# Kernel optimization log

Hardware: AMD Instinct MI355X
Metric: run time of the kernel (lower is better)

## Reference

```python
import jax, jax.numpy as jnp
import numpy as np

TAU = 0.5
EPS = 1e-8


def setup_inputs() -> dict:
    key = jax.random.key(0)
    k1, k2 = jax.random.split(key)
    N, D = 200000, 512
    z_pos = jax.random.normal(k1, (N, D), dtype=jnp.float32)
    W = jax.random.normal(k2, (D, D), dtype=jnp.float32) * (1.0 / np.sqrt(D))
    b = jnp.zeros((D,), dtype=jnp.float32)
    return {"z_pos": z_pos, "W": W, "b": b}


def reference(z_pos, W, b):
    # sample_centroid: softmax-weighted centroid (computed on detached embeddings)
    h = jax.lax.stop_gradient(z_pos)
    init_c = h.mean(axis=0)                              # [D]
    d2 = jnp.sum((h - init_c[None, :]) ** 2, axis=1)     # [N]
    w = jax.nn.softmax(-d2 / TAU)                        # [N]
    c = jnp.sum(h * w[:, None], axis=0)                  # [D]

    # SimNet: dist = 1 - cosine_similarity(proj(x), c)
    x_proj = z_pos @ W.T + b                             # [N, D]
    x_norm = jnp.maximum(jnp.linalg.norm(x_proj, axis=-1), EPS)  # [N]
    c_norm = jnp.maximum(jnp.linalg.norm(c), EPS)
    cos = (x_proj @ c) / (x_norm * c_norm)               # [N]
    dist = 1.0 - cos
    return dist
```

## Files before the change

kernel.cpp:

```cpp
#include <hip/hip_runtime.h>
#include <hip/hip_bf16.h>
#include <math.h>

#define DD 512
#define EPSF 1e-8f
#define BM 64
#define BK 32

typedef __bf16 bf16_t;
typedef __bf16 bf16x4 __attribute__((ext_vector_type(4)));
typedef __bf16 bf16x8 __attribute__((ext_vector_type(8)));
typedef float f32x4 __attribute__((ext_vector_type(4)));

__global__ void k_convW(const float* __restrict__ W, bf16_t* __restrict__ Wb) {
    int i = blockIdx.x * blockDim.x + threadIdx.x;
    float4 v = ((const float4*)W)[i];
    bf16x4 o;
    o[0] = (bf16_t)v.x; o[1] = (bf16_t)v.y; o[2] = (bf16_t)v.z; o[3] = (bf16_t)v.w;
    ((bf16x4*)Wb)[i] = o;
}

__global__ void k_colsum(const float* __restrict__ z, float* __restrict__ part, int N) {
    int t = threadIdx.x;
    int b = blockIdx.x;
    const float2* z2 = (const float2*)z;
    float2 acc = make_float2(0.f, 0.f);
    #pragma unroll 4
    for (int r = b; r < N; r += gridDim.x) {
        float2 v = z2[(size_t)r * (DD / 2) + t];
        acc.x += v.x; acc.y += v.y;
    }
    part[(size_t)b * DD + 2 * t]     = acc.x;
    part[(size_t)b * DD + 2 * t + 1] = acc.y;
}

__global__ void k_wcolsum(const float* __restrict__ z, const float* __restrict__ d2,
                          const float* __restrict__ d2min, const float* __restrict__ sinv,
                          float* __restrict__ part, int N) {
    int t = threadIdx.x;
    int b = blockIdx.x;
    float m  = d2min[0];
    float is = sinv[0];
    const float2* z2 = (const float2*)z;
    float2 acc = make_float2(0.f, 0.f);
    #pragma unroll 2
    for (int r = b; r < N; r += gridDim.x) {
        float w = expf(-2.0f * (d2[r] - m)) * is;
        float2 v = z2[(size_t)r * (DD / 2) + t];
        acc.x += w * v.x; acc.y += w * v.y;
    }
    part[(size_t)b * DD + 2 * t]     = acc.x;
    part[(size_t)b * DD + 2 * t + 1] = acc.y;
}

__global__ void k_reduce1024(const float* __restrict__ part, float* __restrict__ outv, float scale) {
    __shared__ float sm[256];
    int j = blockIdx.x;
    int t = threadIdx.x;
    float s = part[(size_t)t * DD + j] + part[(size_t)(t + 256) * DD + j]
            + part[(size_t)(t + 512) * DD + j] + part[(size_t)(t + 768) * DD + j];
    sm[t] = s;
    __syncthreads();
    for (int st = 128; st > 0; st >>= 1) {
        if (t < st) sm[t] += sm[t + st];
        __syncthreads();
    }
    if (t == 0) outv[j] = sm[0] * scale;
}

__global__ void k_d2(const float* __restrict__ z, const float* __restrict__ cbar,
                     float* __restrict__ d2, int N) {
    int lane = threadIdx.x & 63;
    int gw = (blockIdx.x * blockDim.x + threadIdx.x) >> 6;
    int nw = (gridDim.x * blockDim.x) >> 6;
    const float4* c4 = (const float4*)cbar;
    float4 ca = c4[lane];
    float4 cb = c4[lane + 64];
    for (int r = gw; r < N; r += nw) {
        const float4* zr = (const float4*)(z + (size_t)r * DD);
        float4 a  = zr[lane];
        float4 bb = zr[lane + 64];
        float d, s = 0.f;
        d = a.x  - ca.x; s += d * d;
        d = a.y  - ca.y; s += d * d;
        d = a.z  - ca.z; s += d * d;
        d = a.w  - ca.w; s += d * d;
        d = bb.x - cb.x; s += d * d;
        d = bb.y - cb.y; s += d * d;
        d = bb.z - cb.z; s += d * d;
        d = bb.w - cb.w; s += d * d;
        #pragma unroll
        for (int off = 32; off > 0; off >>= 1) s += __shfl_down(s, off, 64);
        if (lane == 0) d2[r] = s;
    }
}

__global__ void k_min_part(const float* __restrict__ d2, float* __restrict__ outp, int N) {
    __shared__ float sm[256];
    float m = 3.402823466e+38f;
    for (int i = blockIdx.x * blockDim.x + threadIdx.x; i < N; i += gridDim.x * blockDim.x)
        m = fminf(m, d2[i]);
    sm[threadIdx.x] = m;
    __syncthreads();
    for (int s = 128; s > 0; s >>= 1) {
        if (threadIdx.x < s) sm[threadIdx.x] = fminf(sm[threadIdx.x], sm[threadIdx.x + s]);
        __syncthreads();
    }
    if (threadIdx.x == 0) outp[blockIdx.x] = sm[0];
}

__global__ void k_min_final(const float* __restrict__ inp, float* __restrict__ outp) {
    __shared__ float sm[256];
    sm[threadIdx.x] = inp[threadIdx.x];
    __syncthreads();
    for (int s = 128; s > 0; s >>= 1) {
        if (threadIdx.x < s) sm[threadIdx.x] = fminf(sm[threadIdx.x], sm[threadIdx.x + s]);
        __syncthreads();
    }
    if (threadIdx.x == 0) outp[0] = sm[0];
}

__global__ void k_sumexp_part(const float* __restrict__ d2, const float* __restrict__ d2min,
                              float* __restrict__ outp, int N) {
    __shared__ float sm[256];
    float m = d2min[0];
    float s = 0.f;
    for (int i = blockIdx.x * blockDim.x + threadIdx.x; i < N; i += gridDim.x * blockDim.x)
        s += expf(-2.0f * (d2[i] - m));
    sm[threadIdx.x] = s;
    __syncthreads();
    for (int st = 128; st > 0; st >>= 1) {
        if (threadIdx.x < st) sm[threadIdx.x] += sm[threadIdx.x + st];
        __syncthreads();
    }
    if (threadIdx.x == 0) outp[blockIdx.x] = sm[0];
}

__global__ void k_sum_final_inv(const float* __restrict__ inp, float* __restrict__ outp) {
    __shared__ float sm[256];
    sm[threadIdx.x] = inp[threadIdx.x];
    __syncthreads();
    for (int st = 128; st > 0; st >>= 1) {
        if (threadIdx.x < st) sm[threadIdx.x] += sm[threadIdx.x + st];
        __syncthreads();
    }
    if (threadIdx.x == 0) outp[0] = 1.0f / sm[0];
}

__global__ void k_cnorm(const float* __restrict__ cvec, float* __restrict__ outp) {
    __shared__ float sm[512];
    float v = cvec[threadIdx.x];
    sm[threadIdx.x] = v * v;
    __syncthreads();
    for (int st = 256; st > 0; st >>= 1) {
        if (threadIdx.x < st) sm[threadIdx.x] += sm[threadIdx.x + st];
        __syncthreads();
    }
    if (threadIdx.x == 0) outp[0] = 1.0f / fmaxf(sqrtf(sm[0]), EPSF);
}

__global__ __launch_bounds__(512) void k_gemm(
    const float* __restrict__ z, const bf16_t* __restrict__ Wb,
    const float* __restrict__ bvec, const float* __restrict__ cvec,
    const float* __restrict__ cninv, float* __restrict__ out, int N)
{
    __shared__ bf16_t As[BM * BK];
    __shared__ bf16_t Bs[DD * BK];
    __shared__ float psq[BM][4];
    __shared__ float pdt[BM][4];

    const int t    = threadIdx.x;
    const int lane = t & 63;
    const int wv   = t >> 6;
    const int wr   = wv >> 2;
    const int wc   = wv & 3;
    const int quad = lane >> 4;
    const int l15  = lane & 15;
    const int row0 = blockIdx.x * BM;

    const int ai = t >> 3;
    const int aq = t & 7;
    const float4* zsrc = (const float4*)(z + (size_t)(row0 + ai) * DD) + aq;
    const bool arow_ok = (row0 + ai) < N;

    const int bj = t >> 2;
    const int bk = (t & 3) * 8;

    f32x4 acc[2][8];
    #pragma unroll
    for (int a = 0; a < 2; ++a)
        #pragma unroll
        for (int b = 0; b < 8; ++b) acc[a][b] = (f32x4){0.f, 0.f, 0.f, 0.f};

    for (int kc = 0; kc < DD; kc += BK) {
        #pragma unroll
        for (int q = 0; q < 4; ++q) {
            const bf16_t* gp = Wb + (size_t)(q * 128 + bj) * DD + kc + bk;
            int ldsoff = __builtin_amdgcn_readfirstlane(q * 8192 + wv * 1024);
            __builtin_amdgcn_global_load_lds(
                (const __attribute__((address_space(1))) unsigned int*)(const void*)gp,
                (__attribute__((address_space(3))) unsigned int*)(void*)((char*)Bs + ldsoff),
                16, 0, 0);
        }
        float4 v = make_float4(0.f, 0.f, 0.f, 0.f);
        if (arow_ok) v = zsrc[kc >> 2];
        bf16x4 a4;
        a4[0] = (bf16_t)v.x; a4[1] = (bf16_t)v.y; a4[2] = (bf16_t)v.z; a4[3] = (bf16_t)v.w;
        *(bf16x4*)(As + ai * BK + 4 * aq) = a4;

        asm volatile("s_waitcnt vmcnt(0) lgkmcnt(0)" ::: "memory");
        __syncthreads();

        bf16x8 af0 = *(const bf16x8*)(As + (wr * 32 + l15) * BK + quad * 8);
        bf16x8 af1 = *(const bf16x8*)(As + (wr * 32 + 16 + l15) * BK + quad * 8);
        #pragma unroll
        for (int ct = 0; ct < 8; ++ct) {
            bf16x8 bf = *(const bf16x8*)(Bs + (wc * 128 + ct * 16 + l15) * BK + quad * 8);
            acc[0][ct] = __builtin_amdgcn_mfma_f32_16x16x32_bf16(af0, bf, acc[0][ct], 0, 0, 0);
            acc[1][ct] = __builtin_amdgcn_mfma_f32_16x16x32_bf16(af1, bf, acc[1][ct], 0, 0, 0);
        }
        __syncthreads();
    }

    float bc[8], cc[8];
    #pragma unroll
    for (int ct = 0; ct < 8; ++ct) {
        int col = wc * 128 + ct * 16 + l15;
        bc[ct] = bvec[col];
        cc[ct] = cvec[col];
    }
    #pragma unroll
    for (int rt = 0; rt < 2; ++rt) {
        #pragma unroll
        for (int rg = 0; rg < 4; ++rg) {
            float sq = 0.f, dt = 0.f;
            #pragma unroll
            for (int ct = 0; ct < 8; ++ct) {
                float x = acc[rt][ct][rg] + bc[ct];
                sq += x * x;
                dt += x * cc[ct];
            }
            #pragma unroll
            for (int off = 1; off < 16; off <<= 1) {
                sq += __shfl_xor(sq, off, 64);
                dt += __shfl_xor(dt, off, 64);
            }
            if (l15 == 0) {
                int rl = wr * 32 + rt * 16 + quad * 4 + rg;
                psq[rl][wc] = sq;
                pdt[rl][wc] = dt;
            }
        }
    }
    __syncthreads();
    if (t < BM) {
        int r = row0 + t;
        if (r < N) {
            float sq = psq[t][0] + psq[t][1] + psq[t][2] + psq[t][3];
            float dt = pdt[t][0] + pdt[t][1] + pdt[t][2] + pdt[t][3];
            float xi = 1.0f / fmaxf(sqrtf(sq), EPSF);
            out[r] = 1.0f - dt * xi * cninv[0];
        }
    }
}

extern "C" void kernel_launch(void* const* d_in, const int* in_sizes, int n_in,
                              void* d_out, int out_size, void* d_ws, size_t ws_size,
                              hipStream_t stream)
{
    const float* z = (const float*)d_in[0];
    const float* W = (const float*)d_in[1];
    const float* b = (const float*)d_in[2];
    float* out = (float*)d_out;
    int N = in_sizes[0] / DD;

    float* ws = (float*)d_ws;
    size_t off = 0;
    float* part  = ws + off; off += (size_t)1024 * DD;
    float* cbar  = ws + off; off += DD;
    float* d2    = ws + off; off += (size_t)N;
    float* minp  = ws + off; off += 256;
    float* d2min = ws + off; off += 1;
    float* sump  = ws + off; off += 256;
    float* sinv  = ws + off; off += 1;
    float* cvec  = ws + off; off += DD;
    float* cninv = ws + off; off += 1;
    off = (off + 3) & ~(size_t)3;
    bf16_t* Wb   = (bf16_t*)(ws + off);

    k_convW<<<256, 256, 0, stream>>>(W, Wb);
    k_colsum<<<1024, 256, 0, stream>>>(z, part, N);
    k_reduce1024<<<DD, 256, 0, stream>>>(part, cbar, 1.0f / (float)N);
    k_d2<<<1024, 256, 0, stream>>>(z, cbar, d2, N);
    k_min_part<<<256, 256, 0, stream>>>(d2, minp, N);
    k_min_final<<<1, 256, 0, stream>>>(minp, d2min);
    k_sumexp_part<<<256, 256, 0, stream>>>(d2, d2min, sump, N);
    k_sum_final_inv<<<1, 256, 0, stream>>>(sump, sinv);
    k_wcolsum<<<1024, 256, 0, stream>>>(z, d2, d2min, sinv, part, N);
    k_reduce1024<<<DD, 256, 0, stream>>>(part, cvec, 1.0f);
    k_cnorm<<<1, DD, 0, stream>>>(cvec, cninv);
    int nblk = (N + BM - 1) / BM;
    k_gemm<<<nblk, 512, 0, stream>>>(z, Wb, b, cvec, cninv, out, N);
}
```

Measured before the change: 1.004 ms.

## Double-buffer GEMM with larger tile, fuse online softmax stats, widen column sums

The GEMM tile grows to 128 rows and gains double-buffered LDS, so the next K-slice of W and z is loaded while MFMAs run on the current one. Each wave now computes four row tiles, reusing every B fragment across them. The separate min and sum-exp reduction kernels are replaced by an online max/sum-exp computed inside the d2 kernel plus one combine kernel, which removes several launches and passes over d2. The column-sum kernels switch to float4 loads over row pairs with a shared-memory merge. Costs are more registers and LDS per GEMM block, fewer blocks in flight, and a fast-math __expf in the softmax weights.

```diff
diff --git a/kernel.cpp b/kernel.cpp
--- a/kernel.cpp
+++ b/kernel.cpp
@@ -4,8 +4,9 @@
 
 #define DD 512
 #define EPSF 1e-8f
-#define BM 64
+#define BM 128
 #define BK 32
+#define FBIG 3.402823466e+38f
 
 typedef __bf16 bf16_t;
 typedef __bf16 bf16x4 __attribute__((ext_vector_type(4)));
@@ -23,34 +24,56 @@
 __global__ void k_colsum(const float* __restrict__ z, float* __restrict__ part, int N) {
     int t = threadIdx.x;
     int b = blockIdx.x;
-    const float2* z2 = (const float2*)z;
-    float2 acc = make_float2(0.f, 0.f);
-    #pragma unroll 4
-    for (int r = b; r < N; r += gridDim.x) {
-        float2 v = z2[(size_t)r * (DD / 2) + t];
-        acc.x += v.x; acc.y += v.y;
-    }
-    part[(size_t)b * DD + 2 * t]     = acc.x;
-    part[(size_t)b * DD + 2 * t + 1] = acc.y;
+    int col4 = t & 127, sub = t >> 7;
+    const float4* z4 = (const float4*)z;
+    float4 acc = make_float4(0.f, 0.f, 0.f, 0.f);
+    int npair = (N + 1) >> 1;
+    #pragma unroll 2
+    for (int p = b; p < npair; p += gridDim.x) {
+        int r = p * 2 + sub;
+        if (r < N) {
+            float4 v = z4[(size_t)r * 128 + col4];
+            acc.x += v.x; acc.y += v.y; acc.z += v.z; acc.w += v.w;
+        }
+    }
+    __shared__ float4 sm[128];
+    if (sub == 1) sm[col4] = acc;
+    __syncthreads();
+    if (sub == 0) {
+        float4 o = sm[col4];
+        acc.x += o.x; acc.y += o.y; acc.z += o.z; acc.w += o.w;
+        ((float4*)(part + (size_t)b * DD))[col4] = acc;
+    }
 }
 
 __global__ void k_wcolsum(const float* __restrict__ z, const float* __restrict__ d2,
-                          const float* __restrict__ d2min, const float* __restrict__ sinv,
+                          const float* __restrict__ d2min, const float* __restrict__ sinvp,
                           float* __restrict__ part, int N) {
     int t = threadIdx.x;
     int b = blockIdx.x;
+    int col4 = t & 127, sub = t >> 7;
     float m  = d2min[0];
-    float is = sinv[0];
-    const float2* z2 = (const float2*)z;
-    float2 acc = make_float2(0.f, 0.f);
+    float is = sinvp[0];
+    const float4* z4 = (const float4*)z;
+    float4 acc = make_float4(0.f, 0.f, 0.f, 0.f);
+    int npair = (N + 1) >> 1;
     #pragma unroll 2
-    for (int r = b; r < N; r += gridDim.x) {
-        float w = expf(-2.0f * (d2[r] - m)) * is;
-        float2 v = z2[(size_t)r * (DD / 2) + t];
-        acc.x += w * v.x; acc.y += w * v.y;
-    }
-    part[(size_t)b * DD + 2 * t]     = acc.x;
-    part[(size_t)b * DD + 2 * t + 1] = acc.y;
+    for (int p = b; p < npair; p += gridDim.x) {
+        int r = p * 2 + sub;
+        if (r < N) {
+            float w = __expf(-2.0f * (d2[r] - m)) * is;
+            float4 v = z4[(size_t)r * 128 + col4];
+            acc.x += w * v.x; acc.y += w * v.y; acc.z += w * v.z; acc.w += w * v.w;
+        }
+    }
+    __shared__ float4 sm[128];
+    if (sub == 1) sm[col4] = acc;
+    __syncthreads();
+    if (sub == 0) {
+        float4 o = sm[col4];
+        acc.x += o.x; acc.y += o.y; acc.z += o.z; acc.w += o.w;
+        ((float4*)(part + (size_t)b * DD))[col4] = acc;
+    }
 }
 
 __global__ void k_reduce1024(const float* __restrict__ part, float* __restrict__ outv, float scale) {
@@ -68,83 +91,74 @@
     if (t == 0) outv[j] = sm[0] * scale;
 }
 
-__global__ void k_d2(const float* __restrict__ z, const float* __restrict__ cbar,
-                     float* __restrict__ d2, int N) {
+__global__ void k_d2s(const float* __restrict__ z, const float* __restrict__ cbar,
+                      float* __restrict__ d2, float* __restrict__ mpart,
+                      float* __restrict__ spart, int N) {
     int lane = threadIdx.x & 63;
+    int wvid = threadIdx.x >> 6;
     int gw = (blockIdx.x * blockDim.x + threadIdx.x) >> 6;
     int nw = (gridDim.x * blockDim.x) >> 6;
     const float4* c4 = (const float4*)cbar;
     float4 ca = c4[lane];
     float4 cb = c4[lane + 64];
+    float m = FBIG, s = 0.f;
     for (int r = gw; r < N; r += nw) {
         const float4* zr = (const float4*)(z + (size_t)r * DD);
         float4 a  = zr[lane];
         float4 bb = zr[lane + 64];
-        float d, s = 0.f;
-        d = a.x  - ca.x; s += d * d;
-        d = a.y  - ca.y; s += d * d;
-        d = a.z  - ca.z; s += d * d;
-        d = a.w  - ca.w; s += d * d;
-        d = bb.x - cb.x; s += d * d;
-        d = bb.y - cb.y; s += d * d;
-        d = bb.z - cb.z; s += d * d;
-        d = bb.w - cb.w; s += d * d;
-        #pragma unroll
-        for (int off = 32; off > 0; off >>= 1) s += __shfl_down(s, off, 64);
-        if (lane == 0) d2[r] = s;
-    }
-}
-
-__global__ void k_min_part(const float* __restrict__ d2, float* __restrict__ outp, int N) {
-    __shared__ float sm[256];
-    float m = 3.402823466e+38f;
-    for (int i = blockIdx.x * blockDim.x + threadIdx.x; i < N; i += gridDim.x * blockDim.x)
-        m = fminf(m, d2[i]);
-    sm[threadIdx.x] = m;
-    __syncthreads();
-    for (int s = 128; s > 0; s >>= 1) {
-        if (threadIdx.x < s) sm[threadIdx.x] = fminf(sm[threadIdx.x], sm[threadIdx.x + s]);
+        float d, sum = 0.f;
+        d = a.x  - ca.x; sum += d * d;
+        d = a.y  - ca.y; sum += d * d;
+        d = a.z  - ca.z; sum += d * d;
+        d = a.w  - ca.w; sum += d * d;
+        d = bb.x - cb.x; sum += d * d;
+        d = bb.y - cb.y; sum += d * d;
+        d = bb.z - cb.z; sum += d * d;
+        d = bb.w - cb.w; sum += d * d;
+        #pragma unroll
+        for (int off = 1; off < 64; off <<= 1) sum += __shfl_xor(sum, off, 64);
+        if (lane == 0) d2[r] = sum;
+        float nm = fminf(m, sum);
+        s = s * __expf(-2.0f * (m - nm)) + __expf(-2.0f * (sum - nm));
+        m = nm;
+    }
+    __shared__ float smm[4], sms[4];
+    if (lane == 0) { smm[wvid] = m; sms[wvid] = s; }
+    __syncthreads();
+    if (threadIdx.x == 0) {
+        float M = smm[0];
+        M = fminf(M, smm[1]); M = fminf(M, smm[2]); M = fminf(M, smm[3]);
+        float S = 0.f;
+        #pragma unroll
+        for (int i = 0; i < 4; ++i) S += sms[i] * __expf(-2.0f * (smm[i] - M));
+        mpart[blockIdx.x] = M;
+        spart[blockIdx.x] = S;
+    }
+}
+
+__global__ void k_combine(const float* __restrict__ mpart, const float* __restrict__ spart,
+                          float* __restrict__ d2min, float* __restrict__ sinvp) {
+    __shared__ float smm[256], sms[256];
+    int t = threadIdx.x;
+    float M = FBIG, S = 0.f;
+    for (int i = t; i < 1024; i += 256) {
+        float m2 = mpart[i], s2 = spart[i];
+        float nm = fminf(M, m2);
+        S = S * __expf(-2.0f * (M - nm)) + s2 * __expf(-2.0f * (m2 - nm));
+        M = nm;
+    }
+    smm[t] = M; sms[t] = S;
+    __syncthreads();
+    for (int st = 128; st > 0; st >>= 1) {
+        if (t < st) {
+            float m2 = smm[t + st], s2 = sms[t + st];
+            float nm = fminf(smm[t], m2);
+            sms[t] = sms[t] * __expf(-2.0f * (smm[t] - nm)) + s2 * __expf(-2.0f * (m2 - nm));
+            smm[t] = nm;
+        }
         __syncthreads();
     }
-    if (threadIdx.x == 0) outp[blockIdx.x] = sm[0];
-}
-
-__global__ void k_min_final(const float* __restrict__ inp, float* __restrict__ outp) {
-    __shared__ float sm[256];
-    sm[threadIdx.x] = inp[threadIdx.x];
-    __syncthreads();
-    for (int s = 128; s > 0; s >>= 1) {
-        if (threadIdx.x < s) sm[threadIdx.x] = fminf(sm[threadIdx.x], sm[threadIdx.x + s]);
-        __syncthreads();
-    }
-    if (threadIdx.x == 0) outp[0] = sm[0];
-}
-
-__global__ void k_sumexp_part(const float* __restrict__ d2, const float* __restrict__ d2min,
-                              float* __restrict__ outp, int N) {
-    __shared__ float sm[256];
-    float m = d2min[0];
-    float s = 0.f;
-    for (int i = blockIdx.x * blockDim.x + threadIdx.x; i < N; i += gridDim.x * blockDim.x)
-        s += expf(-2.0f * (d2[i] - m));
-    sm[threadIdx.x] = s;
-    __syncthreads();
-    for (int st = 128; st > 0; st >>= 1) {
-        if (threadIdx.x < st) sm[threadIdx.x] += sm[threadIdx.x + st];
-        __syncthreads();
-    }
-    if (threadIdx.x == 0) outp[blockIdx.x] = sm[0];
-}
-
-__global__ void k_sum_final_inv(const float* __restrict__ inp, float* __restrict__ outp) {
-    __shared__ float sm[256];
-    sm[threadIdx.x] = inp[threadIdx.x];
-    __syncthreads();
-    for (int st = 128; st > 0; st >>= 1) {
-        if (threadIdx.x < st) sm[threadIdx.x] += sm[threadIdx.x + st];
-        __syncthreads();
-    }
-    if (threadIdx.x == 0) outp[0] = 1.0f / sm[0];
+    if (t == 0) { d2min[0] = smm[0]; sinvp[0] = 1.0f / sms[0]; }
 }
 
 __global__ void k_cnorm(const float* __restrict__ cvec, float* __restrict__ outp) {
@@ -159,13 +173,13 @@
     if (threadIdx.x == 0) outp[0] = 1.0f / fmaxf(sqrtf(sm[0]), EPSF);
 }
 
-__global__ __launch_bounds__(512) void k_gemm(
+__global__ __launch_bounds__(512, 2) void k_gemm(
     const float* __restrict__ z, const bf16_t* __restrict__ Wb,
     const float* __restrict__ bvec, const float* __restrict__ cvec,
     const float* __restrict__ cninv, float* __restrict__ out, int N)
 {
-    __shared__ bf16_t As[BM * BK];
-    __shared__ bf16_t Bs[DD * BK];
+    __shared__ bf16_t As[2][BM * BK];
+    __shared__ bf16_t Bs[2][DD * BK];
     __shared__ float psq[BM][4];
     __shared__ float pdt[BM][4];
 
@@ -178,47 +192,75 @@
     const int l15  = lane & 15;
     const int row0 = blockIdx.x * BM;
 
-    const int ai = t >> 3;
-    const int aq = t & 7;
-    const float4* zsrc = (const float4*)(z + (size_t)(row0 + ai) * DD) + aq;
+    const int ai = t >> 2;
+    const int ak = (t & 3) * 8;
     const bool arow_ok = (row0 + ai) < N;
-
-    const int bj = t >> 2;
-    const int bk = (t & 3) * 8;
-
-    f32x4 acc[2][8];
+    const float4* zrow = (const float4*)(z + (size_t)(row0 + ai) * DD + ak);
+
+    const bf16_t* bsrc = Wb + (size_t)(t >> 2) * DD + (t & 3) * 8;
+
+    f32x4 acc[4][8];
     #pragma unroll
-    for (int a = 0; a < 2; ++a)
+    for (int a = 0; a < 4; ++a)
         #pragma unroll
         for (int b = 0; b < 8; ++b) acc[a][b] = (f32x4){0.f, 0.f, 0.f, 0.f};
 
-    for (int kc = 0; kc < DD; kc += BK) {
-        #pragma unroll
-        for (int q = 0; q < 4; ++q) {
-            const bf16_t* gp = Wb + (size_t)(q * 128 + bj) * DD + kc + bk;
-            int ldsoff = __builtin_amdgcn_readfirstlane(q * 8192 + wv * 1024);
-            __builtin_amdgcn_global_load_lds(
-                (const __attribute__((address_space(1))) unsigned int*)(const void*)gp,
-                (__attribute__((address_space(3))) unsigned int*)(void*)((char*)Bs + ldsoff),
-                16, 0, 0);
-        }
-        float4 v = make_float4(0.f, 0.f, 0.f, 0.f);
-        if (arow_ok) v = zsrc[kc >> 2];
-        bf16x4 a4;
-        a4[0] = (bf16_t)v.x; a4[1] = (bf16_t)v.y; a4[2] = (bf16_t)v.z; a4[3] = (bf16_t)v.w;
-        *(bf16x4*)(As + ai * BK + 4 * aq) = a4;
-
-        asm volatile("s_waitcnt vmcnt(0) lgkmcnt(0)" ::: "memory");
-        __syncthreads();
-
-        bf16x8 af0 = *(const bf16x8*)(As + (wr * 32 + l15) * BK + quad * 8);
-        bf16x8 af1 = *(const bf16x8*)(As + (wr * 32 + 16 + l15) * BK + quad * 8);
+    #pragma unroll
+    for (int q = 0; q < 4; ++q) {
+        int ldsoff = __builtin_amdgcn_readfirstlane(q * 8192 + wv * 1024);
+        __builtin_amdgcn_global_load_lds(
+            (const __attribute__((address_space(1))) unsigned int*)(const void*)(bsrc + (size_t)q * 128 * DD),
+            (__attribute__((address_space(3))) unsigned int*)(void*)((char*)&Bs[0][0] + ldsoff),
+            16, 0, 0);
+    }
+    {
+        float4 v0 = make_float4(0.f,0.f,0.f,0.f), v1 = v0;
+        if (arow_ok) { v0 = zrow[0]; v1 = zrow[1]; }
+        bf16x8 a8;
+        a8[0]=(bf16_t)v0.x; a8[1]=(bf16_t)v0.y; a8[2]=(bf16_t)v0.z; a8[3]=(bf16_t)v0.w;
+        a8[4]=(bf16_t)v1.x; a8[5]=(bf16_t)v1.y; a8[6]=(bf16_t)v1.z; a8[7]=(bf16_t)v1.w;
+        *(bf16x8*)(&As[0][ai * BK + ak]) = a8;
+    }
+    asm volatile("s_waitcnt vmcnt(0)" ::: "memory");
+    __syncthreads();
+
+    #pragma unroll 1
+    for (int kc2 = 0; kc2 < 16; ++kc2) {
+        const int cur = kc2 & 1;
+        const int nxt = cur ^ 1;
+        float4 v0 = make_float4(0.f,0.f,0.f,0.f), v1 = v0;
+        if (kc2 < 15) {
+            const int kc = (kc2 + 1) * BK;
+            #pragma unroll
+            for (int q = 0; q < 4; ++q) {
+                int ldsoff = __builtin_amdgcn_readfirstlane(q * 8192 + wv * 1024);
+                __builtin_amdgcn_global_load_lds(
+                    (const __attribute__((address_space(1))) unsigned int*)(const void*)(bsrc + (size_t)q * 128 * DD + kc),
+                    (__attribute__((address_space(3))) unsigned int*)(void*)((char*)&Bs[nxt][0] + ldsoff),
+                    16, 0, 0);
+            }
+            if (arow_ok) { v0 = zrow[kc >> 2]; v1 = zrow[(kc >> 2) + 1]; }
+        }
+
+        bf16x8 af[4];
+        #pragma unroll
+        for (int rt = 0; rt < 4; ++rt)
+            af[rt] = *(const bf16x8*)(&As[cur][(wr * 64 + rt * 16 + l15) * BK + quad * 8]);
         #pragma unroll
         for (int ct = 0; ct < 8; ++ct) {
-            bf16x8 bf = *(const bf16x8*)(Bs + (wc * 128 + ct * 16 + l15) * BK + quad * 8);
-            acc[0][ct] = __builtin_amdgcn_mfma_f32_16x16x32_bf16(af0, bf, acc[0][ct], 0, 0, 0);
-            acc[1][ct] = __builtin_amdgcn_mfma_f32_16x16x32_bf16(af1, bf, acc[1][ct], 0, 0, 0);
-        }
+            bf16x8 bfv = *(const bf16x8*)(&Bs[cur][(wc * 128 + ct * 16 + l15) * BK + quad * 8]);
+            #pragma unroll
+            for (int rt = 0; rt < 4; ++rt)
+                acc[rt][ct] = __builtin_amdgcn_mfma_f32_16x16x32_bf16(af[rt], bfv, acc[rt][ct], 0, 0, 0);
+        }
+
+        if (kc2 < 15) {
+            bf16x8 a8;
+            a8[0]=(bf16_t)v0.x; a8[1]=(bf16_t)v0.y; a8[2]=(bf16_t)v0.z; a8[3]=(bf16_t)v0.w;
+            a8[4]=(bf16_t)v1.x; a8[5]=(bf16_t)v1.y; a8[6]=(bf16_t)v1.z; a8[7]=(bf16_t)v1.w;
+            *(bf16x8*)(&As[nxt][ai * BK + ak]) = a8;
+        }
+        asm volatile("s_waitcnt vmcnt(0)" ::: "memory");
         __syncthreads();
     }
 
@@ -230,7 +272,7 @@
         cc[ct] = cvec[col];
     }
     #pragma unroll
-    for (int rt = 0; rt < 2; ++rt) {
+    for (int rt = 0; rt < 4; ++rt) {
         #pragma unroll
         for (int rg = 0; rg < 4; ++rg) {
             float sq = 0.f, dt = 0.f;
@@ -246,7 +288,7 @@
                 dt += __shfl_xor(dt, off, 64);
             }
             if (l15 == 0) {
-                int rl = wr * 32 + rt * 16 + quad * 4 + rg;
+                int rl = wr * 64 + rt * 16 + quad * 4 + rg;
                 psq[rl][wc] = sq;
                 pdt[rl][wc] = dt;
             }
@@ -279,10 +321,10 @@
     float* part  = ws + off; off += (size_t)1024 * DD;
     float* cbar  = ws + off; off += DD;
     float* d2    = ws + off; off += (size_t)N;
-    float* minp  = ws + off; off += 256;
+    float* mpart = ws + off; off += 1024;
+    float* spart = ws + off; off += 1024;
     float* d2min = ws + off; off += 1;
-    float* sump  = ws + off; off += 256;
-    float* sinv  = ws + off; off += 1;
+    float* sinvp = ws + off; off += 1;
     float* cvec  = ws + off; off += DD;
     float* cninv = ws + off; off += 1;
     off = (off + 3) & ~(size_t)3;
@@ -291,12 +333,9 @@
     k_convW<<<256, 256, 0, stream>>>(W, Wb);
     k_colsum<<<1024, 256, 0, stream>>>(z, part, N);
     k_reduce1024<<<DD, 256, 0, stream>>>(part, cbar, 1.0f / (float)N);
-    k_d2<<<1024, 256, 0, stream>>>(z, cbar, d2, N);
-    k_min_part<<<256, 256, 0, stream>>>(d2, minp, N);
-    k_min_final<<<1, 256, 0, stream>>>(minp, d2min);
-    k_sumexp_part<<<256, 256, 0, stream>>>(d2, d2min, sump, N);
-    k_sum_final_inv<<<1, 256, 0, stream>>>(sump, sinv);
-    k_wcolsum<<<1024, 256, 0, stream>>>(z, d2, d2min, sinv, part, N);
+    k_d2s<<<1024, 256, 0, stream>>>(z, cbar, d2, mpart, spart, N);
+    k_combine<<<1, 256, 0, stream>>>(mpart, spart, d2min, sinvp);
+    k_wcolsum<<<1024, 256, 0, stream>>>(z, d2, d2min, sinvp, part, N);
     k_reduce1024<<<DD, 256, 0, stream>>>(part, cvec, 1.0f);
     k_cnorm<<<1, DD, 0, stream>>>(cvec, cninv);
     int nblk = (N + BM - 1) / BM;
```

After: 931.4 us. 1.08x faster.
